# Kernel tuning notes

Hardware: AMD Instinct MI355X
Metric: run time of the kernel (lower is better)

The kernel has to match this reference:

```python
import jax, jax.numpy as jnp
import numpy as np

S, B, C = 14, 2, 20          # grid size, boxes per cell, classes
LAMBDA_COORD, LAMBDA_NOOBJ = 5.0, 0.5
NCH = 5 * B + C              # 30 channels


def setup_inputs() -> dict:
    key = jax.random.key(0)
    k1, k2, k3 = jax.random.split(key, 3)
    Nb = 4096
    # positive values: loss takes sqrt(w), sqrt(h)
    pred = jax.random.uniform(k1, (Nb, S, S, NCH), dtype=jnp.float32, minval=0.05, maxval=1.0)
    target = jax.random.uniform(k2, (Nb, S, S, NCH), dtype=jnp.float32, minval=0.05, maxval=1.0)
    # binarize conf channels so coord (conf>0) / noobj (conf==0) partition the cells
    objf = (jax.random.uniform(k3, (Nb, S, S)) < 0.3).astype(jnp.float32)
    for b in range(B):
        target = target.at[..., 4 + 5 * b].set(objf)
    return {"pred_tensor": pred, "target_tensor": target}


def _to_xyxy(box):
    # box [..., 5] (or [..., B, 5]): cell-relative x,y and global w,h -> corners
    xy = box[..., :2] / S
    half = 0.5 * box[..., 2:4]
    return jnp.concatenate([xy - half, xy + half], axis=-1)


def reference(pred_tensor, target_tensor):
    pred, target = pred_tensor, target_tensor
    obj = (target[..., 4] > 0).astype(pred.dtype)      # [Nb,S,S]
    noobj = (target[..., 4] == 0).astype(pred.dtype)   # [Nb,S,S]

    pb = pred[..., :5 * B].reshape(pred.shape[:3] + (B, 5))     # [Nb,S,S,B,5]
    tb = target[..., :5 * B].reshape(target.shape[:3] + (B, 5))  # [Nb,S,S,B,5]

    # no-object confidence loss: conf channel of every box slot in noobj cells
    loss_noobj = jnp.sum(noobj[..., None] * (pb[..., 4] - tb[..., 4]) ** 2)

    # IoU of each of B predicted boxes vs the (first) target box of the cell
    pxy = _to_xyxy(pb)                        # [Nb,S,S,B,4]
    txy = _to_xyxy(tb[..., 0, :])[..., None, :]  # [Nb,S,S,1,4]
    lt = jnp.maximum(pxy[..., :2], txy[..., :2])
    rb = jnp.minimum(pxy[..., 2:], txy[..., 2:])
    wh = jnp.clip(rb - lt, 0.0)
    inter = wh[..., 0] * wh[..., 1]           # [Nb,S,S,B]
    area_p = (pxy[..., 2] - pxy[..., 0]) * (pxy[..., 3] - pxy[..., 1])
    area_t = (txy[..., 2] - txy[..., 0]) * (txy[..., 3] - txy[..., 1])
    iou = inter / (area_p + area_t - inter)

    max_iou = jax.lax.stop_gradient(jnp.max(iou, axis=-1))  # torch uses .data (detach)
    r = jnp.argmax(iou, axis=-1)              # responsible box index [Nb,S,S]

    pr = jnp.take_along_axis(pb, r[..., None, None], axis=3)[..., 0, :]  # [Nb,S,S,5]
    tr = jnp.take_along_axis(tb, r[..., None, None], axis=3)[..., 0, :]

    m = obj
    loss_xy = jnp.sum(m[..., None] * (pr[..., :2] - tr[..., :2]) ** 2)
    # guard sqrt in masked-out cells (values there don't matter)
    safe_pwh = jnp.where(m[..., None] > 0, pr[..., 2:4], 1.0)
    safe_twh = jnp.where(m[..., None] > 0, tr[..., 2:4], 1.0)
    loss_wh = jnp.sum(m[..., None] * (jnp.sqrt(safe_pwh) - jnp.sqrt(safe_twh)) ** 2)
    loss_obj = jnp.sum(m * (pr[..., 4] - max_iou) ** 2)
    loss_class = jnp.sum(m[..., None] * (pred[..., 5 * B:] - target[..., 5 * B:]) ** 2)

    loss = LAMBDA_COORD * (loss_xy + loss_wh) + loss_obj + LAMBDA_NOOBJ * loss_noobj + loss_class
    return loss / pred.shape[0]
```

## Files before the change

kernel.cpp:

```cpp
#include <hip/hip_runtime.h>


#define NB 4096
#define NCELL (NB * 14 * 14)
#define NCH 30
#define CHUNK_CELLS 128
#define CHUNKS_PER_BLOCK 8
#define CELLS_PER_BLOCK (CHUNK_CELLS * CHUNKS_PER_BLOCK)
#define NBLOCKS (NCELL / CELLS_PER_BLOCK)
#define CHUNK_FLOATS (CHUNK_CELLS * NCH)
#define CHUNK_F4 (CHUNK_FLOATS / 4)

#define GLOBAL_AS __attribute__((address_space(1)))
#define LDS_AS    __attribute__((address_space(3)))

__device__ __forceinline__ void async_copy16(const float* g, float* l) {
    __builtin_amdgcn_global_load_lds((const GLOBAL_AS void*)g, (LDS_AS void*)l,
                                     16, 0, 0);
}

__device__ __forceinline__ void stage_chunk(const float* __restrict__ pred,
                                            const float* __restrict__ target,
                                            float* pbuf, float* tbuf,
                                            size_t cellbase, int tid)
{
    const float* gp = pred + cellbase * NCH;
    const float* gt = target + cellbase * NCH;
#pragma unroll
    for (int r = 0; r < 4; ++r) {
        int idx = r * 256 + tid;
        if (idx < CHUNK_F4) {
            async_copy16(gp + (size_t)idx * 4, pbuf + idx * 4);
            async_copy16(gt + (size_t)idx * 4, tbuf + idx * 4);
        }
    }
}

__device__ __forceinline__ float cell_loss_lds(const float* __restrict__ pl,
                                               const float* __restrict__ tl)
{
    const float2* p2 = (const float2*)pl;
    const float2* t2 = (const float2*)tl;

    float p[10], t[10];
#pragma unroll
    for (int i = 0; i < 5; ++i) {
        float2 a = p2[i]; p[2 * i] = a.x; p[2 * i + 1] = a.y;
        float2 b = t2[i]; t[2 * i] = b.x; t[2 * i + 1] = b.y;
    }

    const float t4 = t[4];
    const bool obj = (t4 > 0.0f);

    float dn0 = p[4] - t[4];
    float dn1 = p[9] - t[9];
    float noobj_l = (t4 == 0.0f) ? (dn0 * dn0 + dn1 * dn1) : 0.0f;

    const float invS = 1.0f / 14.0f;
    float tcx = t[0] * invS, tcy = t[1] * invS;
    float tx1 = tcx - 0.5f * t[2], ty1 = tcy - 0.5f * t[3];
    float tx2 = tcx + 0.5f * t[2], ty2 = tcy + 0.5f * t[3];
    float area_t = (tx2 - tx1) * (ty2 - ty1);

    float iou[2];
#pragma unroll
    for (int b = 0; b < 2; ++b) {
        const float* pb = p + 5 * b;
        float cx = pb[0] * invS, cy = pb[1] * invS;
        float x1 = cx - 0.5f * pb[2], y1 = cy - 0.5f * pb[3];
        float x2 = cx + 0.5f * pb[2], y2 = cy + 0.5f * pb[3];
        float lx = fmaxf(x1, tx1), ly = fmaxf(y1, ty1);
        float rx = fminf(x2, tx2), ry = fminf(y2, ty2);
        float wx = fmaxf(rx - lx, 0.0f), wy = fmaxf(ry - ly, 0.0f);
        float inter = wx * wy;
        float area_p = (x2 - x1) * (y2 - y1);
        iou[b] = inter / (area_p + area_t - inter);
    }

    const bool r = (iou[1] > iou[0]);
    float max_iou = fmaxf(iou[0], iou[1]);

    float pr0 = r ? p[5] : p[0], tr0 = r ? t[5] : t[0];
    float pr1 = r ? p[6] : p[1], tr1 = r ? t[6] : t[1];
    float pr2 = r ? p[7] : p[2], tr2 = r ? t[7] : t[2];
    float pr3 = r ? p[8] : p[3], tr3 = r ? t[8] : t[3];
    float pr4 = r ? p[9] : p[4];

    float lcls = 0.0f;
#pragma unroll
    for (int i = 5; i < 15; ++i) {
        float2 a = p2[i];
        float2 b = t2[i];
        float d0 = a.x - b.x, d1 = a.y - b.y;
        lcls += d0 * d0 + d1 * d1;
    }

    float obj_l = 0.0f;
    if (obj) {
        float dx = pr0 - tr0, dy = pr1 - tr1;
        float lxy = dx * dx + dy * dy;
        float dw = sqrtf(pr2) - sqrtf(tr2);
        float dh = sqrtf(pr3) - sqrtf(tr3);
        float lwh = dw * dw + dh * dh;
        float dob = pr4 - max_iou;
        float lob = dob * dob;
        obj_l = 5.0f * (lxy + lwh) + lob + lcls;
    }
    return obj_l + 0.5f * noobj_l;
}

__global__ __launch_bounds__(256) void yolo_loss_partial(
    const float* __restrict__ pred, const float* __restrict__ target,
    float* __restrict__ partial)
{
    __shared__ __align__(16) float buf[2][2][CHUNK_FLOATS];
    __shared__ float red[4];

    const int tid = threadIdx.x;
    const size_t blockcell = (size_t)blockIdx.x * CELLS_PER_BLOCK;

    stage_chunk(pred, target, buf[0][0], buf[0][1], blockcell, tid);
    __syncthreads();

    float acc = 0.0f;
    for (int c = 0; c < CHUNKS_PER_BLOCK; ++c) {
        const int cur = c & 1;
        if (c + 1 < CHUNKS_PER_BLOCK)
            stage_chunk(pred, target, buf[cur ^ 1][0], buf[cur ^ 1][1],
                        blockcell + (size_t)(c + 1) * CHUNK_CELLS, tid);
        if (tid < CHUNK_CELLS)
            acc += cell_loss_lds(&buf[cur][0][tid * NCH],
                                 &buf[cur][1][tid * NCH]);
        __syncthreads();
    }

    float v = acc;
#pragma unroll
    for (int off = 32; off > 0; off >>= 1)
        v += __shfl_down(v, off, 64);

    const int lane = threadIdx.x & 63;
    const int wid = threadIdx.x >> 6;
    if (lane == 0) red[wid] = v;
    __syncthreads();
    if (threadIdx.x == 0)
        partial[blockIdx.x] = red[0] + red[1] + red[2] + red[3];
}

__global__ __launch_bounds__(256) void yolo_loss_finalize(
    const float* __restrict__ partial, float* __restrict__ out)
{
    double s = 0.0;
    for (int i = threadIdx.x; i < NBLOCKS; i += 256)
        s += (double)partial[i];

    __shared__ double sh[256];
    sh[threadIdx.x] = s;
    __syncthreads();
#pragma unroll
    for (int step = 128; step > 0; step >>= 1) {
        if (threadIdx.x < step) sh[threadIdx.x] += sh[threadIdx.x + step];
        __syncthreads();
    }
    if (threadIdx.x == 0)
        out[0] = (float)(sh[0] / (double)NB);
}

extern "C" void kernel_launch(void* const* d_in, const int* in_sizes, int n_in,
                              void* d_out, int out_size, void* d_ws, size_t ws_size,
                              hipStream_t stream) {
    const float* pred = (const float*)d_in[0];
    const float* target = (const float*)d_in[1];
    float* out = (float*)d_out;
    float* partial = (float*)d_ws;

    yolo_loss_partial<<<NBLOCKS, 256, 0, stream>>>(pred, target, partial);
    yolo_loss_finalize<<<1, 256, 0, stream>>>(partial, out);
}
```

Measured before the change: 214.6 us.

## Switch to single-wave blocks with split vmcnt waits over staged LDS

Replaces the 256-thread, double-buffered, 8-chunk block loop with one-wavefront blocks that each stage a single 128-cell tile of pred and target into LDS through direct global-to-LDS loads. The wave computes the first 64 cells as soon as the first 16 loads have landed (s_waitcnt vmcnt(14)), then waits for the rest before the second 64 cells. This removes block-level barriers, idle threads, and the cross-wave reduction. Smaller LDS footprint per block lets more independent blocks keep loads in flight per CU. In exchange there are many more blocks and partials for the finalize pass to sum, and correctness depends on the hand-placed vmcnt counts matching the in-order load issue.

```diff
diff --git a/kernel.cpp b/kernel.cpp
--- a/kernel.cpp
+++ b/kernel.cpp
@@ -4,36 +4,16 @@
 #define NB 4096
 #define NCELL (NB * 14 * 14)
 #define NCH 30
-#define CHUNK_CELLS 128
-#define CHUNKS_PER_BLOCK 8
-#define CELLS_PER_BLOCK (CHUNK_CELLS * CHUNKS_PER_BLOCK)
-#define NBLOCKS (NCELL / CELLS_PER_BLOCK)
-#define CHUNK_FLOATS (CHUNK_CELLS * NCH)
-#define CHUNK_F4 (CHUNK_FLOATS / 4)
+#define WAVE_CELLS 128
+#define NBLOCKS (NCELL / WAVE_CELLS)
+#define SEG 1024
 
 #define GLOBAL_AS __attribute__((address_space(1)))
 #define LDS_AS    __attribute__((address_space(3)))
 
-__device__ __forceinline__ void async_copy16(const float* g, float* l) {
+__device__ __forceinline__ void async16(const char* g, char* l) {
     __builtin_amdgcn_global_load_lds((const GLOBAL_AS void*)g, (LDS_AS void*)l,
                                      16, 0, 0);
-}
-
-__device__ __forceinline__ void stage_chunk(const float* __restrict__ pred,
-                                            const float* __restrict__ target,
-                                            float* pbuf, float* tbuf,
-                                            size_t cellbase, int tid)
-{
-    const float* gp = pred + cellbase * NCH;
-    const float* gt = target + cellbase * NCH;
-#pragma unroll
-    for (int r = 0; r < 4; ++r) {
-        int idx = r * 256 + tid;
-        if (idx < CHUNK_F4) {
-            async_copy16(gp + (size_t)idx * 4, pbuf + idx * 4);
-            async_copy16(gt + (size_t)idx * 4, tbuf + idx * 4);
-        }
-    }
 }
 
 __device__ __forceinline__ float cell_loss_lds(const float* __restrict__ pl,
@@ -109,42 +89,41 @@
     return obj_l + 0.5f * noobj_l;
 }
 
-__global__ __launch_bounds__(256) void yolo_loss_partial(
+__global__ __launch_bounds__(64) void yolo_loss_partial(
     const float* __restrict__ pred, const float* __restrict__ target,
     float* __restrict__ partial)
 {
-    __shared__ __align__(16) float buf[2][2][CHUNK_FLOATS];
-    __shared__ float red[4];
+    __shared__ __align__(16) float pbuf[WAVE_CELLS * NCH];
+    __shared__ __align__(16) float tbuf[WAVE_CELLS * NCH];
 
-    const int tid = threadIdx.x;
-    const size_t blockcell = (size_t)blockIdx.x * CELLS_PER_BLOCK;
+    const int lane = threadIdx.x;
+    const size_t base = (size_t)blockIdx.x * WAVE_CELLS * NCH;
+    const char* gp = (const char*)(pred + base);
+    const char* gt = (const char*)(target + base);
+    char* lp = (char*)pbuf;
+    char* lt = (char*)tbuf;
+    const int lo = lane * 16;
 
-    stage_chunk(pred, target, buf[0][0], buf[0][1], blockcell, tid);
-    __syncthreads();
+#pragma unroll
+    for (int r = 0; r < 15; ++r) {
+        async16(gp + r * SEG + lo, lp + r * SEG + lo);
+        async16(gt + r * SEG + lo, lt + r * SEG + lo);
+    }
 
-    float acc = 0.0f;
-    for (int c = 0; c < CHUNKS_PER_BLOCK; ++c) {
-        const int cur = c & 1;
-        if (c + 1 < CHUNKS_PER_BLOCK)
-            stage_chunk(pred, target, buf[cur ^ 1][0], buf[cur ^ 1][1],
-                        blockcell + (size_t)(c + 1) * CHUNK_CELLS, tid);
-        if (tid < CHUNK_CELLS)
-            acc += cell_loss_lds(&buf[cur][0][tid * NCH],
-                                 &buf[cur][1][tid * NCH]);
-        __syncthreads();
-    }
+    asm volatile("s_waitcnt vmcnt(14)" ::: "memory");
+    __builtin_amdgcn_sched_barrier(0);
+    float acc = cell_loss_lds(pbuf + lane * NCH, tbuf + lane * NCH);
+
+    asm volatile("s_waitcnt vmcnt(0)" ::: "memory");
+    __builtin_amdgcn_sched_barrier(0);
+    acc += cell_loss_lds(pbuf + (64 + lane) * NCH, tbuf + (64 + lane) * NCH);
 
     float v = acc;
 #pragma unroll
     for (int off = 32; off > 0; off >>= 1)
         v += __shfl_down(v, off, 64);
-
-    const int lane = threadIdx.x & 63;
-    const int wid = threadIdx.x >> 6;
-    if (lane == 0) red[wid] = v;
-    __syncthreads();
-    if (threadIdx.x == 0)
-        partial[blockIdx.x] = red[0] + red[1] + red[2] + red[3];
+    if (lane == 0)
+        partial[blockIdx.x] = v;
 }
 
 __global__ __launch_bounds__(256) void yolo_loss_finalize(
@@ -174,6 +153,6 @@
     float* out = (float*)d_out;
     float* partial = (float*)d_ws;
 
-    yolo_loss_partial<<<NBLOCKS, 256, 0, stream>>>(pred, target, partial);
+    yolo_loss_partial<<<NBLOCKS, 64, 0, stream>>>(pred, target, partial);
     yolo_loss_finalize<<<1, 256, 0, stream>>>(partial, out);
 }
```

Result: no change. 211.4 us (-1.5%).
